# Kernel optimization log

Measured on AMD Instinct MI355X. Metric: run time of the kernel, lower is better.

Reference implementation:

```python
import jax, jax.numpy as jnp
import numpy as np

N, C, H, W = 4, 256, 32, 32
NH = 2                      # att_nhead
HD = C // NH                # 128 per-head dim
MAX_DIS = 7
WS = 2 * MAX_DIS + 1        # 15 window side
WW = WS * WS                # 225 window positions
T = (C / NH) ** 0.5


def _gather_idx(h, w):
    # idx[wpos, m]: flat index into zero-padded (h+14, w+14) grid of the
    # neighbor at window offset wpos for query pixel m (== F.unfold semantics)
    pw = w + 2 * MAX_DIS
    dy, dx = np.meshgrid(np.arange(WS), np.arange(WS), indexing='ij')
    ys, xs = np.meshgrid(np.arange(h), np.arange(w), indexing='ij')
    idx = (dy.reshape(-1, 1) + ys.reshape(1, -1)) * pw + (dx.reshape(-1, 1) + xs.reshape(1, -1))
    return jnp.asarray(idx, dtype=jnp.int32)  # [WW, h*w]


def setup_inputs() -> dict:
    key = jax.random.key(0)
    ks = jax.random.split(key, 14)
    s = 0.02
    return {
        'q': jax.random.normal(ks[0], (N, C, H, W), jnp.float32),
        'k': jax.random.normal(ks[1], (N, C, H, W), jnp.float32),
        'v': jax.random.normal(ks[2], (N, C, H, W), jnp.float32),
        'Wq': jax.random.normal(ks[3], (C, C), jnp.float32) * s,
        'bq': jnp.zeros((C,), jnp.float32),
        'Wk': jax.random.normal(ks[4], (C, C), jnp.float32) * s,
        'bk': jnp.zeros((C,), jnp.float32),
        'Wv': jax.random.normal(ks[5], (C, C), jnp.float32) * s,
        'bv': jnp.zeros((C,), jnp.float32),
        'Wrel': jax.random.normal(ks[6], (NH, WW, HD), jnp.float32) * s,   # grouped 1x1 conv
        'brel': jnp.zeros((NH * WW,), jnp.float32),
        'V_bias': jax.random.normal(ks[7], (NH, HD, WW), jnp.float32) * s,
        'Wfc': jax.random.normal(ks[8], (C, C), jnp.float32) * s,
        'bfc': jnp.zeros((C,), jnp.float32),
    }


def _conv1x1(x, Wt, b):
    return jnp.einsum('nchw,dc->ndhw', x, Wt) + b[None, :, None, None]


def reference(q, k, v, Wq, bq, Wk, bk, Wv, bv, Wrel, brel, V_bias, Wfc, bfc):
    n, c, h, w = q.shape
    hw = h * w
    idx = _gather_idx(h, w)                                   # [WW, hw]
    pad = ((0, 0), (0, 0), (0, 0), (MAX_DIS, MAX_DIS), (MAX_DIS, MAX_DIS))

    q = _conv1x1(q, Wq, bq)
    k = _conv1x1(k, Wk, bk)
    v = _conv1x1(v, Wv, bv)

    # grouped 1x1 conv: relative position logits, [n, NH, WW, hw]
    rel = jnp.einsum('ngcxy,gwc->ngwxy', q.reshape(n, NH, HD, h, w), Wrel)
    rel = rel + brel.reshape(NH, WW)[None, :, :, None, None]
    rel = rel.reshape(n, NH, WW, hw)

    qs = (q / T).reshape(n, NH, HD, hw)

    # unfold K via zero-pad + gather: [n, NH, HD, WW, hw]
    k_pad = jnp.pad(k.reshape(n, NH, HD, h, w), pad).reshape(n, NH, HD, -1)
    k_un = k_pad[..., idx]
    qk = jnp.einsum('ngcm,ngcwm->ngwm', qs, k_un) + rel

    # boundary mask: neighbor inside the original image
    valid = jnp.pad(jnp.ones((h, w), jnp.float32), MAX_DIS).reshape(-1)[idx] > 0
    qk = jnp.where(valid[None, None], qk, jnp.float32(-1e8))
    attn = jax.nn.softmax(qk, axis=2)                         # over window positions

    agg_bias = jnp.einsum('ngwm,gcw->mngc', attn, V_bias).reshape(hw, n, c)

    # local2global scatter + dense einsum == gather of zero-padded V
    v_pad = jnp.pad(v.reshape(n, NH, HD, h, w), pad).reshape(n, NH, HD, -1)
    v_un = v_pad[..., idx]                                    # [n, NH, HD, WW, hw]
    agg_value = jnp.einsum('ngwm,ngcwm->mngc', attn, v_un).reshape(hw, n, c)

    out = (agg_value + agg_bias) @ Wfc.T + bfc                # [hw, n, c]
    return out
```

## Files before the change

kernel.cpp:

```cpp
#include <hip/hip_runtime.h>
#include <math.h>


typedef __attribute__((ext_vector_type(8))) short short8;
typedef __attribute__((ext_vector_type(4))) float floatx4;

__device__ __forceinline__ short f2bf(float f) {
    unsigned u = __float_as_uint(f);
    unsigned r = (u + 0x7fffu + ((u >> 16) & 1u)) >> 16;
    return (short)r;
}
__device__ __forceinline__ float bf2f(short s) {
    return __uint_as_float(((unsigned)(unsigned short)s) << 16);
}

__global__ __launch_bounds__(256)
void conv_kernel(const float* __restrict__ q, const float* __restrict__ k,
                 const float* __restrict__ v,
                 const float* __restrict__ Wq, const float* __restrict__ Wk,
                 const float* __restrict__ Wv, const float* __restrict__ Wfc,
                 const float* __restrict__ Wrel,
                 short* __restrict__ Xhi, short* __restrict__ Xlo,
                 short* __restrict__ Whi, short* __restrict__ Wlo,
                 short* __restrict__ Wrh, short* __restrict__ Wrl)
{
    const int tid = threadIdx.x;
    const int z = blockIdx.z;
    const int lane = tid & 63;
    const int n16 = lane & 15, quad = lane >> 4;

    if (z < 12) {
        __shared__ float st[64 * 33];
        const int sel = z >> 2, batch = z & 3;
        const float* X = (sel == 0 ? q : sel == 1 ? k : v) + ((long)batch << 18);
        const int mb = blockIdx.x, kc = blockIdx.y;
#pragma unroll
        for (int it = 0; it < 8; ++it) {
            int e = tid + it * 256;
            int cc = e >> 6, mm = e & 63;
            st[mm * 33 + cc] = X[((long)(kc * 32 + cc) << 10) + mb * 64 + mm];
        }
        __syncthreads();
        const int mtl = tid >> 6;
        const int m = mtl * 16 + n16;
        short h[8], l[8];
#pragma unroll
        for (int j = 0; j < 8; ++j) {
            float f = st[m * 33 + quad * 8 + j];
            short hb = f2bf(f);
            h[j] = hb;
            l[j] = f2bf(f - bf2f(hb));
        }
        int mt16 = mb * 4 + mtl;
        long off = (long)z * 262144 + (((long)(mt16 * 8 + kc) * 64) + lane) * 8;
        *(short8*)(Xhi + off) = *(short8*)&h[0];
        *(short8*)(Xlo + off) = *(short8*)&l[0];
    } else if (z < 16) {
        if (tid >= 64) return;
        const int w = z - 12;
        const float* W = (w == 0 ? Wq : w == 1 ? Wk : w == 2 ? Wv : Wfc);
        const int dt = blockIdx.x, kc = blockIdx.y;
        const int d = dt * 16 + n16, cb = kc * 32 + quad * 8;
        float4 w0 = *(const float4*)&W[d * 256 + cb];
        float4 w1 = *(const float4*)&W[d * 256 + cb + 4];
        float f[8] = {w0.x, w0.y, w0.z, w0.w, w1.x, w1.y, w1.z, w1.w};
        short h[8], l[8];
#pragma unroll
        for (int j = 0; j < 8; ++j) {
            short hb = f2bf(f[j]);
            h[j] = hb;
            l[j] = f2bf(f[j] - bf2f(hb));
        }
        long off = (long)w * 65536 + (((long)(dt * 8 + kc) * 64) + lane) * 8;
        *(short8*)(Whi + off) = *(short8*)&h[0];
        *(short8*)(Wlo + off) = *(short8*)&l[0];
    } else {
        if (tid >= 64) return;
        const int g = z - 16;
        const int wt = blockIdx.x, kc = blockIdx.y;
        if (wt >= 15 || kc >= 4) return;
        const int w = wt * 16 + n16;
        const int cb = kc * 32 + quad * 8;
        float f[8] = {0.f, 0.f, 0.f, 0.f, 0.f, 0.f, 0.f, 0.f};
        if (w < 225) {
            float4 w0 = *(const float4*)&Wrel[(long)(g * 225 + w) * 128 + cb];
            float4 w1 = *(const float4*)&Wrel[(long)(g * 225 + w) * 128 + cb + 4];
            f[0] = w0.x; f[1] = w0.y; f[2] = w0.z; f[3] = w0.w;
            f[4] = w1.x; f[5] = w1.y; f[6] = w1.z; f[7] = w1.w;
        }
        short h[8], l[8];
#pragma unroll
        for (int j = 0; j < 8; ++j) {
            short hb = f2bf(f[j]);
            h[j] = hb;
            l[j] = f2bf(f[j] - bf2f(hb));
        }
        long off = (long)g * 30720 + (((long)(wt * 4 + kc) * 64) + lane) * 8;
        *(short8*)(Wrh + off) = *(short8*)&h[0];
        *(short8*)(Wrl + off) = *(short8*)&l[0];
    }
}

__global__ __launch_bounds__(256)
void mfma_proj(const short* __restrict__ Xhi, const short* __restrict__ Xlo,
               const short* __restrict__ Whi, const short* __restrict__ Wlo,
               const float* __restrict__ bq, const float* __restrict__ bk,
               const float* __restrict__ bv,
               short* __restrict__ qhi, short* __restrict__ qlo,
               short* __restrict__ khi, short* __restrict__ klo,
               float* __restrict__ vpad)
{
    __shared__ float tile[64 * 65];
    const int tid = threadIdx.x;
    const int wave = tid >> 6, lane = tid & 63;
    const int n16 = lane & 15, quad = lane >> 4;
    const int mb = blockIdx.x, db = blockIdx.y, z = blockIdx.z;
    const int sel = z >> 2, batch = z & 3;
    const int dt = db * 4 + wave;

    const short* Ah = Whi + (long)sel * 65536 + ((long)(dt * 8) * 64 + lane) * 8;
    const short* Al = Wlo + (long)sel * 65536 + ((long)(dt * 8) * 64 + lane) * 8;
    short8 ahi[8], alo[8];
#pragma unroll
    for (int kc = 0; kc < 8; ++kc) {
        ahi[kc] = *(const short8*)(Ah + kc * 512);
        alo[kc] = *(const short8*)(Al + kc * 512);
    }
    const short* Bh = Xhi + (long)z * 262144;
    const short* Bl = Xlo + (long)z * 262144;

    const float* bias = (sel == 0 ? bq : sel == 1 ? bk : bv);
    float4 bv4 = *(const float4*)&bias[dt * 16 + quad * 4];
    float bb[4] = {bv4.x, bv4.y, bv4.z, bv4.w};

    if (sel == 2) {
#pragma unroll
        for (int mtl = 0; mtl < 4; ++mtl) {
            const int mt16 = mb * 4 + mtl;
            floatx4 acc = {0.f, 0.f, 0.f, 0.f};
#pragma unroll
            for (int kc = 0; kc < 8; ++kc) {
                long bo = ((long)(mt16 * 8 + kc) * 64 + lane) * 8;
                short8 bh = *(const short8*)(Bh + bo);
                short8 bl = *(const short8*)(Bl + bo);
                acc = __builtin_amdgcn_mfma_f32_16x16x32_bf16(ahi[kc], bh, acc, 0, 0, 0);
                acc = __builtin_amdgcn_mfma_f32_16x16x32_bf16(ahi[kc], bl, acc, 0, 0, 0);
                acc = __builtin_amdgcn_mfma_f32_16x16x32_bf16(alo[kc], bh, acc, 0, 0, 0);
            }
            const int m = mt16 * 16 + n16;
            float* Y = vpad + (long)batch * 393216;
            const int row = m >> 5, col = (m & 31) + 8;
#pragma unroll
            for (int r = 0; r < 4; ++r)
                Y[(long)(dt * 16 + quad * 4 + r) * 1536 + row * 48 + col] = acc[r] + bb[r];
        }
        return;
    }

#pragma unroll
    for (int mtl = 0; mtl < 4; ++mtl) {
        const int mt16 = mb * 4 + mtl;
        floatx4 acc = {0.f, 0.f, 0.f, 0.f};
#pragma unroll
        for (int kc = 0; kc < 8; ++kc) {
            long bo = ((long)(mt16 * 8 + kc) * 64 + lane) * 8;
            short8 bh = *(const short8*)(Bh + bo);
            short8 bl = *(const short8*)(Bl + bo);
            acc = __builtin_amdgcn_mfma_f32_16x16x32_bf16(ahi[kc], bh, acc, 0, 0, 0);
            acc = __builtin_amdgcn_mfma_f32_16x16x32_bf16(ahi[kc], bl, acc, 0, 0, 0);
            acc = __builtin_amdgcn_mfma_f32_16x16x32_bf16(alo[kc], bh, acc, 0, 0, 0);
        }
        const int ml = mtl * 16 + n16;
        const int cl = wave * 16 + quad * 4;
#pragma unroll
        for (int r = 0; r < 4; ++r)
            tile[ml * 65 + cl + r] = acc[r] + bb[r];
    }
    __syncthreads();

    const float scale = (sel == 1) ? 0.08838834764831845f : 1.0f;
    const int m_l = tid >> 2, c16 = (tid & 3) * 16;
    const int m = mb * 64 + m_l;
    const int cglob = db * 64 + c16;
    const int g = cglob >> 7, ch = cglob & 127;
    const long base = (((long)(batch * 2 + g) << 10) + m) * 128 + ch;
    short h[16], l[16];
#pragma unroll
    for (int j = 0; j < 16; ++j) {
        float f = tile[m_l * 65 + c16 + j] * scale;
        short hb = f2bf(f);
        h[j] = hb;
        l[j] = f2bf(f - bf2f(hb));
    }
    short* oh = sel ? khi : qhi;
    short* ol = sel ? klo : qlo;
    *(short8*)(oh + base)     = *(short8*)&h[0];
    *(short8*)(oh + base + 8) = *(short8*)&h[8];
    *(short8*)(ol + base)     = *(short8*)&l[0];
    *(short8*)(ol + base + 8) = *(short8*)&l[8];
}

__global__ __launch_bounds__(256)
void scores_mfma(const short* __restrict__ qhi, const short* __restrict__ qlo,
                 const short* __restrict__ khi, const short* __restrict__ klo,
                 const short* __restrict__ Wrh, const short* __restrict__ Wrl,
                 const float* __restrict__ brel, float* __restrict__ attn)
{
    __shared__ float qk[16 * 241];
    __shared__ float invl[16];

    const int tid = threadIdx.x;
    const int wave = tid >> 6, lane = tid & 63;
    const int y  = blockIdx.x >> 1;
    const int xt = blockIdx.x & 1;
    const int bz = blockIdx.y;
    const int g = bz & 1;
    const int x0 = xt * 16;
    float* relh = attn + (long)bz * 230400;

    const int n16 = lane & 15, quad = lane >> 4;
    const long qbase = (((long)bz << 10) + y * 32 + x0 + n16) * 128 + quad * 8;
    short8 a_hi[4], a_lo[4];
#pragma unroll
    for (int ch = 0; ch < 4; ++ch) {
        a_hi[ch] = *(const short8*)(qhi + qbase + ch * 32);
        a_lo[ch] = *(const short8*)(qlo + qbase + ch * 32);
    }

    for (int wt = wave; wt < 15; wt += 4) {
        const short* Ah = Wrh + (long)g * 30720 + ((long)(wt * 4) * 64 + lane) * 8;
        const short* Al = Wrl + (long)g * 30720 + ((long)(wt * 4) * 64 + lane) * 8;
        floatx4 racc = {0.f, 0.f, 0.f, 0.f};
#pragma unroll
        for (int kc = 0; kc < 4; ++kc) {
            short8 whh = *(const short8*)(Ah + kc * 512);
            short8 wll = *(const short8*)(Al + kc * 512);
            racc = __builtin_amdgcn_mfma_f32_16x16x32_bf16(whh, a_hi[kc], racc, 0, 0, 0);
            racc = __builtin_amdgcn_mfma_f32_16x16x32_bf16(whh, a_lo[kc], racc, 0, 0, 0);
            racc = __builtin_amdgcn_mfma_f32_16x16x32_bf16(wll, a_hi[kc], racc, 0, 0, 0);
        }
#pragma unroll
        for (int r = 0; r < 4; ++r) {
            int w = wt * 16 + quad * 4 + r;
            if (w < 225) {
                int dy = w / 15, dx = w - dy * 15;
                qk[n16 * 241 + dy * 16 + dx] = racc[r] + brel[g * 225 + w];
            }
        }
    }
    __syncthreads();

    for (int e = tid; e < 16 * 241; e += 256) {
        int px = e / 241, idx = e - px * 241;
        int dy = idx >> 4, dx = idx & 15;
        int hy = y + dy - 7, hx = x0 + px + dx - 7;
        bool valid = (dx < 15) && (dy < 15) &&
                     (hy >= 0) && (hy < 32) && (hx >= 0) && (hx < 32);
        if (!valid) qk[e] = -1e8f;
    }
    __syncthreads();

    for (int dy = wave; dy < 15; dy += 4) {
        const int ky = y + dy - 7;
        if (ky < 0 || ky > 31) continue;
#pragma unroll
        for (int kxt = 0; kxt < 2; ++kxt) {
            const int kxg = x0 - 8 + kxt * 16 + n16;
            const long kb = (((long)bz << 10) + ky * 32 + kxg) * 128 + quad * 8;
            floatx4 acc = {0.f, 0.f, 0.f, 0.f};
#pragma unroll
            for (int ch = 0; ch < 4; ++ch) {
                short8 b_hi = *(const short8*)(khi + kb + ch * 32);
                short8 b_lo = *(const short8*)(klo + kb + ch * 32);
                acc = __builtin_amdgcn_mfma_f32_16x16x32_bf16(a_hi[ch], b_hi, acc, 0, 0, 0);
                acc = __builtin_amdgcn_mfma_f32_16x16x32_bf16(a_hi[ch], b_lo, acc, 0, 0, 0);
                acc = __builtin_amdgcn_mfma_f32_16x16x32_bf16(a_lo[ch], b_hi, acc, 0, 0, 0);
            }
            if (kxg >= 0 && kxg < 32) {
#pragma unroll
                for (int r = 0; r < 4; ++r) {
                    int m = quad * 4 + r;
                    int dx = kxg - (x0 + m) + 7;
                    if (dx >= 0 && dx < 15) {
                        int s = m * 241 + dy * 16 + dx;
                        qk[s] = qk[s] + acc[r];
                    }
                }
            }
        }
    }
    __syncthreads();

    {
        int px = tid >> 4, s = tid & 15;
        float mx = -3.0e38f;
        for (int w = s; w < 240; w += 16) mx = fmaxf(mx, qk[px * 241 + w]);
#pragma unroll
        for (int msk = 8; msk; msk >>= 1) mx = fmaxf(mx, __shfl_xor(mx, msk));
        float sum = 0.f;
        for (int w = s; w < 240; w += 16) {
            float p = __expf(qk[px * 241 + w] - mx);
            qk[px * 241 + w] = p;
            sum += p;
        }
#pragma unroll
        for (int msk = 8; msk; msk >>= 1) sum += __shfl_xor(sum, msk);
        if (s == 0) invl[px] = 1.0f / sum;
    }
    __syncthreads();

    for (int e = tid; e < 3600; e += 256) {
        int px = e & 15, w = e >> 4;
        int dy2 = w / 15, dx2 = w - dy2 * 15;
        relh[((long)w << 10) + y * 32 + x0 + px] =
            qk[px * 241 + dy2 * 16 + dx2] * invl[px];
    }
}

__global__ __launch_bounds__(256)
void pv_kernel(const float* __restrict__ vpad, const float* __restrict__ attn,
               const float* __restrict__ Vbias,
               short* __restrict__ AGhi, short* __restrict__ AGlo)
{
    __shared__ __align__(16) float pa[225 * 32];
    const int tid = threadIdx.x;
    const int y   = blockIdx.x;
    const int chh = blockIdx.y;
    const int bz  = blockIdx.z;
    const int n = bz >> 1, g = bz & 1;

    const float* ab = attn + (long)bz * 230400 + y * 32;
    for (int e = tid; e < 1800; e += 256) {
        int w = e >> 3, x4 = (e & 7) * 4;
        *(float4*)&pa[w * 32 + x4] = *(const float4*)&ab[((long)w << 10) + x4];
    }
    __syncthreads();

    const int chg = tid >> 3;
    const int xq  = tid & 7;
    const int c0  = chh * 64 + chg * 2;
    const int x0  = xq * 4;
    const float* v0 = vpad + (long)bz * 196608 + (long)c0 * 1536;
    const float* v1 = v0 + 1536;
    const float* b0 = Vbias + (g * 128 + c0) * 225;
    const float* b1 = b0 + 225;

    float acc0[4] = {0.f, 0.f, 0.f, 0.f};
    float acc1[4] = {0.f, 0.f, 0.f, 0.f};

    for (int dy = 0; dy < 15; ++dy) {
        int hy = y + dy - 7;
        if (hy < 0 || hy > 31) continue;
        const float4* r0 = (const float4*)(v0 + hy * 48 + x0);
        const float4* r1 = (const float4*)(v1 + hy * 48 + x0);
        float wa[20], wb[20];
#pragma unroll
        for (int t = 0; t < 5; ++t) {
            float4 a = r0[t], b = r1[t];
            wa[4*t+0] = a.x; wa[4*t+1] = a.y; wa[4*t+2] = a.z; wa[4*t+3] = a.w;
            wb[4*t+0] = b.x; wb[4*t+1] = b.y; wb[4*t+2] = b.z; wb[4*t+3] = b.w;
        }
        const float* par = &pa[dy * 15 * 32 + x0];
        const float* vb0 = b0 + dy * 15;
        const float* vb1 = b1 + dy * 15;
#pragma unroll
        for (int dx = 0; dx < 15; ++dx) {
            float4 p4 = *(const float4*)&par[dx * 32];
            float ba = vb0[dx], bb = vb1[dx];
            acc0[0] += p4.x * (wa[1 + dx] + ba);
            acc0[1] += p4.y * (wa[2 + dx] + ba);
            acc0[2] += p4.z * (wa[3 + dx] + ba);
            acc0[3] += p4.w * (wa[4 + dx] + ba);
            acc1[0] += p4.x * (wb[1 + dx] + bb);
            acc1[1] += p4.y * (wb[2 + dx] + bb);
            acc1[2] += p4.z * (wb[3 + dx] + bb);
            acc1[3] += p4.w * (wb[4 + dx] + bb);
        }
    }
    __syncthreads();

    float* tile = pa;
#pragma unroll
    for (int i = 0; i < 4; ++i) {
        tile[(x0 + i) * 65 + chg * 2 + 0] = acc0[i];
        tile[(x0 + i) * 65 + chg * 2 + 1] = acc1[i];
    }
    __syncthreads();

    const int lane = tid & 63, sub = tid >> 6;
    const int kcp = sub & 1, mtp = sub >> 1;
    const int n16 = lane & 15, quad = lane >> 4;
    const int m_loc = mtp * 16 + n16;
    const int c_loc = kcp * 32 + quad * 8;
    short h[8], l[8];
#pragma unroll
    for (int j = 0; j < 8; ++j) {
        float f = tile[m_loc * 65 + c_loc + j];
        short hb = f2bf(f);
        h[j] = hb;
        l[j] = f2bf(f - bf2f(hb));
    }
    const int mt16 = y * 2 + mtp;
    const int kc = g * 4 + chh * 2 + kcp;
    long off = (long)n * 262144 + (((long)(mt16 * 8 + kc) * 64) + lane) * 8;
    *(short8*)(AGhi + off) = *(short8*)&h[0];
    *(short8*)(AGlo + off) = *(short8*)&l[0];
}

__global__ __launch_bounds__(256)
void mfma_fc(const short* __restrict__ Ahi, const short* __restrict__ Alo,
             const short* __restrict__ Whi, const short* __restrict__ Wlo,
             const float* __restrict__ bfc, float* __restrict__ out)
{
    __shared__ float tile[64 * 68];
    const int tid = threadIdx.x;
    const int wave = tid >> 6, lane = tid & 63;
    const int n16 = lane & 15, quad = lane >> 4;
    const int mb = blockIdx.x, db = blockIdx.y, nz = blockIdx.z;
    const int dt = db * 4 + wave;

    const short* Ah = Whi + (long)3 * 65536 + ((long)(dt * 8) * 64 + lane) * 8;
    const short* Al = Wlo + (long)3 * 65536 + ((long)(dt * 8) * 64 + lane) * 8;
    short8 ahi[8], alo[8];
#pragma unroll
    for (int kc = 0; kc < 8; ++kc) {
        ahi[kc] = *(const short8*)(Ah + kc * 512);
        alo[kc] = *(const short8*)(Al + kc * 512);
    }
    const short* Bh = Ahi + (long)nz * 262144;
    const short* Bl = Alo + (long)nz * 262144;

    float4 bv4 = *(const float4*)&bfc[dt * 16 + quad * 4];
    float bb[4] = {bv4.x, bv4.y, bv4.z, bv4.w};

#pragma unroll
    for (int mtl = 0; mtl < 4; ++mtl) {
        const int mt16 = mb * 4 + mtl;
        floatx4 acc = {0.f, 0.f, 0.f, 0.f};
#pragma unroll
        for (int kc = 0; kc < 8; ++kc) {
            long bo = ((long)(mt16 * 8 + kc) * 64 + lane) * 8;
            short8 bh = *(const short8*)(Bh + bo);
            short8 bl = *(const short8*)(Bl + bo);
            acc = __builtin_amdgcn_mfma_f32_16x16x32_bf16(ahi[kc], bh, acc, 0, 0, 0);
            acc = __builtin_amdgcn_mfma_f32_16x16x32_bf16(ahi[kc], bl, acc, 0, 0, 0);
            acc = __builtin_amdgcn_mfma_f32_16x16x32_bf16(alo[kc], bh, acc, 0, 0, 0);
        }
        const int ml = mtl * 16 + n16;
        const int dl = wave * 16 + quad * 4;
#pragma unroll
        for (int r = 0; r < 4; ++r)
            tile[ml * 68 + dl + r] = acc[r] + bb[r];
    }
    __syncthreads();
#pragma unroll
    for (int it = 0; it < 16; ++it) {
        int e = tid + it * 256;
        int dd = e & 63, mm = e >> 6;
        out[(long)(mb * 64 + mm) * 1024 + nz * 256 + db * 64 + dd] = tile[mm * 68 + dd];
    }
}

extern "C" void kernel_launch(void* const* d_in, const int* in_sizes, int n_in,
                              void* d_out, int out_size, void* d_ws, size_t ws_size,
                              hipStream_t stream)
{
    const float* q    = (const float*)d_in[0];
    const float* k    = (const float*)d_in[1];
    const float* v    = (const float*)d_in[2];
    const float* Wq   = (const float*)d_in[3];
    const float* bq   = (const float*)d_in[4];
    const float* Wk   = (const float*)d_in[5];
    const float* bk   = (const float*)d_in[6];
    const float* Wv   = (const float*)d_in[7];
    const float* bv   = (const float*)d_in[8];
    const float* Wrel = (const float*)d_in[9];
    const float* brel = (const float*)d_in[10];
    const float* Vb   = (const float*)d_in[11];
    const float* Wfc  = (const float*)d_in[12];
    const float* bfc  = (const float*)d_in[13];
    float* out = (float*)d_out;

    float* ws   = (float*)d_ws;
    float* vpad = ws + 2097152;
    float* attn = ws + 4718592;
    short* qhi  = (short*)(ws + 6561792);
    short* qlo  = (short*)(ws + 7086080);
    short* khi  = (short*)(ws + 7610368);
    short* klo  = (short*)(ws + 8134656);
    short* Xhi  = (short*)(ws + 8658944);
    short* Xlo  = (short*)(ws + 10231808);
    short* Whi  = (short*)(ws + 11804672);
    short* Wlo  = (short*)(ws + 11935744);
    short* AGhi = (short*)(ws + 12066816);
    short* AGlo = (short*)(ws + 12591104);
    short* Wrh  = (short*)(ws + 13115392);
    short* Wrl  = (short*)(ws + 13146112);

    dim3 blk(256);

    hipMemsetAsync(vpad, 0, (size_t)1572864 * 4, stream);

    conv_kernel<<<dim3(16, 8, 18), blk, 0, stream>>>(q, k, v, Wq, Wk, Wv, Wfc,
                                                     Wrel, Xhi, Xlo, Whi, Wlo,
                                                     Wrh, Wrl);

    mfma_proj<<<dim3(16, 4, 12), blk, 0, stream>>>(Xhi, Xlo, Whi, Wlo,
                                                   bq, bk, bv,
                                                   qhi, qlo, khi, klo, vpad);

    scores_mfma<<<dim3(64, 8), blk, 0, stream>>>(qhi, qlo, khi, klo,
                                                 Wrh, Wrl, brel, attn);

    pv_kernel<<<dim3(32, 2, 8), blk, 0, stream>>>(vpad, attn, Vb, AGhi, AGlo);

    mfma_fc<<<dim3(16, 4, 4), blk, 0, stream>>>(AGhi, AGlo, Whi, Wlo, bfc, out);
}
```

Measured before the change: 174.0 us.

## Fuse softmax scores with PV aggregation and zero V padding in projection

Merges the scores/softmax kernel and the PV aggregation kernel into one launch. Normalized attention now stays in shared memory instead of a global attn buffer written and re-read. Each block now covers 16 pixels and all 128 channels of one head rather than 32 pixels and 64 channels, which changes the per-block work balance. The padding columns of vpad are zeroed inside the projection kernel, replacing a separate full memset.

```diff
diff --git a/kernel.cpp b/kernel.cpp
--- a/kernel.cpp
+++ b/kernel.cpp
@@ -154,6 +154,15 @@
             for (int r = 0; r < 4; ++r)
                 Y[(long)(dt * 16 + quad * 4 + r) * 1536 + row * 48 + col] = acc[r] + bb[r];
         }
+        {
+            float* Y = vpad + (long)batch * 393216;
+            const int ch_l = tid >> 2, rest = tid & 3;
+            const int prow = rest >> 1, side = rest & 1;
+            long po = (long)(db * 64 + ch_l) * 1536 + (mb * 2 + prow) * 48 + side * 40;
+            float4 z4 = make_float4(0.f, 0.f, 0.f, 0.f);
+            *(float4*)&Y[po] = z4;
+            *(float4*)&Y[po + 4] = z4;
+        }
         return;
     }
 
@@ -201,12 +210,15 @@
 }
 
 __global__ __launch_bounds__(256)
-void scores_mfma(const short* __restrict__ qhi, const short* __restrict__ qlo,
-                 const short* __restrict__ khi, const short* __restrict__ klo,
-                 const short* __restrict__ Wrh, const short* __restrict__ Wrl,
-                 const float* __restrict__ brel, float* __restrict__ attn)
+void scores_pv(const short* __restrict__ qhi, const short* __restrict__ qlo,
+               const short* __restrict__ khi, const short* __restrict__ klo,
+               const short* __restrict__ Wrh, const short* __restrict__ Wrl,
+               const float* __restrict__ brel,
+               const float* __restrict__ vpad, const float* __restrict__ Vbias,
+               short* __restrict__ AGhi, short* __restrict__ AGlo)
 {
     __shared__ float qk[16 * 241];
+    __shared__ __align__(16) float pa[225 * 16];
     __shared__ float invl[16];
 
     const int tid = threadIdx.x;
@@ -214,9 +226,8 @@
     const int y  = blockIdx.x >> 1;
     const int xt = blockIdx.x & 1;
     const int bz = blockIdx.y;
-    const int g = bz & 1;
+    const int n = bz >> 1, g = bz & 1;
     const int x0 = xt * 16;
-    float* relh = attn + (long)bz * 230400;
 
     const int n16 = lane & 15, quad = lane >> 4;
     const long qbase = (((long)bz << 10) + y * 32 + x0 + n16) * 128 + quad * 8;
@@ -312,34 +323,15 @@
     for (int e = tid; e < 3600; e += 256) {
         int px = e & 15, w = e >> 4;
         int dy2 = w / 15, dx2 = w - dy2 * 15;
-        relh[((long)w << 10) + y * 32 + x0 + px] =
-            qk[px * 241 + dy2 * 16 + dx2] * invl[px];
-    }
-}
-
-__global__ __launch_bounds__(256)
-void pv_kernel(const float* __restrict__ vpad, const float* __restrict__ attn,
-               const float* __restrict__ Vbias,
-               short* __restrict__ AGhi, short* __restrict__ AGlo)
-{
-    __shared__ __align__(16) float pa[225 * 32];
-    const int tid = threadIdx.x;
-    const int y   = blockIdx.x;
-    const int chh = blockIdx.y;
-    const int bz  = blockIdx.z;
-    const int n = bz >> 1, g = bz & 1;
-
-    const float* ab = attn + (long)bz * 230400 + y * 32;
-    for (int e = tid; e < 1800; e += 256) {
-        int w = e >> 3, x4 = (e & 7) * 4;
-        *(float4*)&pa[w * 32 + x4] = *(const float4*)&ab[((long)w << 10) + x4];
-    }
-    __syncthreads();
-
-    const int chg = tid >> 3;
-    const int xq  = tid & 7;
-    const int c0  = chh * 64 + chg * 2;
-    const int x0  = xq * 4;
+        pa[w * 16 + px] = qk[px * 241 + dy2 * 16 + dx2] * invl[px];
+    }
+    __syncthreads();
+
+    const int chg = tid >> 2;
+    const int xq  = tid & 3;
+    const int c0  = chg * 2;
+    const int x0l = xq * 4;
+    const int x0g = x0 + x0l;
     const float* v0 = vpad + (long)bz * 196608 + (long)c0 * 1536;
     const float* v1 = v0 + 1536;
     const float* b0 = Vbias + (g * 128 + c0) * 225;
@@ -351,8 +343,8 @@
     for (int dy = 0; dy < 15; ++dy) {
         int hy = y + dy - 7;
         if (hy < 0 || hy > 31) continue;
-        const float4* r0 = (const float4*)(v0 + hy * 48 + x0);
-        const float4* r1 = (const float4*)(v1 + hy * 48 + x0);
+        const float4* r0 = (const float4*)(v0 + hy * 48 + x0g);
+        const float4* r1 = (const float4*)(v1 + hy * 48 + x0g);
         float wa[20], wb[20];
 #pragma unroll
         for (int t = 0; t < 5; ++t) {
@@ -360,12 +352,12 @@
             wa[4*t+0] = a.x; wa[4*t+1] = a.y; wa[4*t+2] = a.z; wa[4*t+3] = a.w;
             wb[4*t+0] = b.x; wb[4*t+1] = b.y; wb[4*t+2] = b.z; wb[4*t+3] = b.w;
         }
-        const float* par = &pa[dy * 15 * 32 + x0];
+        const float* par = &pa[dy * 15 * 16 + x0l];
         const float* vb0 = b0 + dy * 15;
         const float* vb1 = b1 + dy * 15;
 #pragma unroll
         for (int dx = 0; dx < 15; ++dx) {
-            float4 p4 = *(const float4*)&par[dx * 32];
+            float4 p4 = *(const float4*)&par[dx * 16];
             float ba = vb0[dx], bb = vb1[dx];
             acc0[0] += p4.x * (wa[1 + dx] + ba);
             acc0[1] += p4.y * (wa[2 + dx] + ba);
@@ -379,29 +371,26 @@
     }
     __syncthreads();
 
-    float* tile = pa;
+    float* tile = qk;
 #pragma unroll
     for (int i = 0; i < 4; ++i) {
-        tile[(x0 + i) * 65 + chg * 2 + 0] = acc0[i];
-        tile[(x0 + i) * 65 + chg * 2 + 1] = acc1[i];
-    }
-    __syncthreads();
-
-    const int lane = tid & 63, sub = tid >> 6;
-    const int kcp = sub & 1, mtp = sub >> 1;
-    const int n16 = lane & 15, quad = lane >> 4;
-    const int m_loc = mtp * 16 + n16;
+        tile[(x0l + i) * 129 + c0 + 0] = acc0[i];
+        tile[(x0l + i) * 129 + c0 + 1] = acc1[i];
+    }
+    __syncthreads();
+
+    const int kcp = tid >> 6;
     const int c_loc = kcp * 32 + quad * 8;
     short h[8], l[8];
 #pragma unroll
     for (int j = 0; j < 8; ++j) {
-        float f = tile[m_loc * 65 + c_loc + j];
+        float f = tile[n16 * 129 + c_loc + j];
         short hb = f2bf(f);
         h[j] = hb;
         l[j] = f2bf(f - bf2f(hb));
     }
-    const int mt16 = y * 2 + mtp;
-    const int kc = g * 4 + chh * 2 + kcp;
+    const int mt16 = y * 2 + xt;
+    const int kc = g * 4 + kcp;
     long off = (long)n * 262144 + (((long)(mt16 * 8 + kc) * 64) + lane) * 8;
     *(short8*)(AGhi + off) = *(short8*)&h[0];
     *(short8*)(AGlo + off) = *(short8*)&l[0];
@@ -483,7 +472,6 @@
 
     float* ws   = (float*)d_ws;
     float* vpad = ws + 2097152;
-    float* attn = ws + 4718592;
     short* qhi  = (short*)(ws + 6561792);
     short* qlo  = (short*)(ws + 7086080);
     short* khi  = (short*)(ws + 7610368);
@@ -499,8 +487,6 @@
 
     dim3 blk(256);
 
-    hipMemsetAsync(vpad, 0, (size_t)1572864 * 4, stream);
-
     conv_kernel<<<dim3(16, 8, 18), blk, 0, stream>>>(q, k, v, Wq, Wk, Wv, Wfc,
                                                      Wrel, Xhi, Xlo, Whi, Wlo,
                                                      Wrh, Wrl);
@@ -509,10 +495,9 @@
                                                    bq, bk, bv,
                                                    qhi, qlo, khi, klo, vpad);
 
-    scores_mfma<<<dim3(64, 8), blk, 0, stream>>>(qhi, qlo, khi, klo,
-                                                 Wrh, Wrl, brel, attn);
-
-    pv_kernel<<<dim3(32, 2, 8), blk, 0, stream>>>(vpad, attn, Vb, AGhi, AGlo);
+    scores_pv<<<dim3(64, 8), blk, 0, stream>>>(qhi, qlo, khi, klo,
+                                               Wrh, Wrl, brel, vpad, Vb,
+                                               AGhi, AGlo);
 
     mfma_fc<<<dim3(16, 4, 4), blk, 0, stream>>>(AGhi, AGlo, Whi, Wlo, bfc, out);
 }
```

Result: slower. 178.1 us (+2.4%).

## Split projection and FC GEMMs into 16-row blocks and drop vpad memset

Applied to the files above, without the earlier changes.

The mfma_proj and mfma_fc kernels now give each block a single 16-row M tile instead of four. The grid grows fourfold, and weight fragments are loaded inside the k-loop instead of held in 16 register vectors. The FC epilogue becomes one float4 store per thread, and the q/k epilogue writes 4-element vectors. The separate hipMemsetAsync on the padded V buffer is removed; the V-projection blocks now write zeros into the horizontal padding columns themselves. The aim is better occupancy and one less memset. The cost is reloading weights once per M tile, plus smaller, less efficient stores.

```diff
diff --git a/kernel.cpp b/kernel.cpp
--- a/kernel.cpp
+++ b/kernel.cpp
@@ -3,6 +3,7 @@
 
 
 typedef __attribute__((ext_vector_type(8))) short short8;
+typedef __attribute__((ext_vector_type(4))) short short4v;
 typedef __attribute__((ext_vector_type(4))) float floatx4;
 
 __device__ __forceinline__ short f2bf(float f) {
@@ -110,22 +111,16 @@
                short* __restrict__ khi, short* __restrict__ klo,
                float* __restrict__ vpad)
 {
-    __shared__ float tile[64 * 65];
+    __shared__ float tile[16 * 65];
     const int tid = threadIdx.x;
     const int wave = tid >> 6, lane = tid & 63;
     const int n16 = lane & 15, quad = lane >> 4;
-    const int mb = blockIdx.x, db = blockIdx.y, z = blockIdx.z;
+    const int mt16 = blockIdx.x, db = blockIdx.y, z = blockIdx.z;
     const int sel = z >> 2, batch = z & 3;
     const int dt = db * 4 + wave;
 
     const short* Ah = Whi + (long)sel * 65536 + ((long)(dt * 8) * 64 + lane) * 8;
     const short* Al = Wlo + (long)sel * 65536 + ((long)(dt * 8) * 64 + lane) * 8;
-    short8 ahi[8], alo[8];
-#pragma unroll
-    for (int kc = 0; kc < 8; ++kc) {
-        ahi[kc] = *(const short8*)(Ah + kc * 512);
-        alo[kc] = *(const short8*)(Al + kc * 512);
-    }
     const short* Bh = Xhi + (long)z * 262144;
     const short* Bl = Xlo + (long)z * 262144;
 
@@ -133,60 +128,51 @@
     float4 bv4 = *(const float4*)&bias[dt * 16 + quad * 4];
     float bb[4] = {bv4.x, bv4.y, bv4.z, bv4.w};
 
+    floatx4 acc = {0.f, 0.f, 0.f, 0.f};
+#pragma unroll
+    for (int kc = 0; kc < 8; ++kc) {
+        short8 ahi = *(const short8*)(Ah + kc * 512);
+        short8 alo = *(const short8*)(Al + kc * 512);
+        long bo = ((long)(mt16 * 8 + kc) * 64 + lane) * 8;
+        short8 bh = *(const short8*)(Bh + bo);
+        short8 bl = *(const short8*)(Bl + bo);
+        acc = __builtin_amdgcn_mfma_f32_16x16x32_bf16(ahi, bh, acc, 0, 0, 0);
+        acc = __builtin_amdgcn_mfma_f32_16x16x32_bf16(ahi, bl, acc, 0, 0, 0);
+        acc = __builtin_amdgcn_mfma_f32_16x16x32_bf16(alo, bh, acc, 0, 0, 0);
+    }
+
     if (sel == 2) {
-#pragma unroll
-        for (int mtl = 0; mtl < 4; ++mtl) {
-            const int mt16 = mb * 4 + mtl;
-            floatx4 acc = {0.f, 0.f, 0.f, 0.f};
-#pragma unroll
-            for (int kc = 0; kc < 8; ++kc) {
-                long bo = ((long)(mt16 * 8 + kc) * 64 + lane) * 8;
-                short8 bh = *(const short8*)(Bh + bo);
-                short8 bl = *(const short8*)(Bl + bo);
-                acc = __builtin_amdgcn_mfma_f32_16x16x32_bf16(ahi[kc], bh, acc, 0, 0, 0);
-                acc = __builtin_amdgcn_mfma_f32_16x16x32_bf16(ahi[kc], bl, acc, 0, 0, 0);
-                acc = __builtin_amdgcn_mfma_f32_16x16x32_bf16(alo[kc], bh, acc, 0, 0, 0);
-            }
-            const int m = mt16 * 16 + n16;
-            float* Y = vpad + (long)batch * 393216;
-            const int row = m >> 5, col = (m & 31) + 8;
-#pragma unroll
-            for (int r = 0; r < 4; ++r)
-                Y[(long)(dt * 16 + quad * 4 + r) * 1536 + row * 48 + col] = acc[r] + bb[r];
+        const int m = mt16 * 16 + n16;
+        float* Y = vpad + (long)batch * 393216;
+        const int row = m >> 5, col = (m & 31) + 8;
+#pragma unroll
+        for (int r = 0; r < 4; ++r)
+            Y[(long)(dt * 16 + quad * 4 + r) * 1536 + row * 48 + col] = acc[r] + bb[r];
+        {
+            const int prow = mt16 >> 1, side = mt16 & 1;
+            const int ch_l = tid >> 2, f2 = (tid & 3) * 2;
+            long po = (long)(db * 64 + ch_l) * 1536 + prow * 48 + side * 40 + f2;
+            Y[po] = 0.f;
+            Y[po + 1] = 0.f;
         }
         return;
     }
 
-#pragma unroll
-    for (int mtl = 0; mtl < 4; ++mtl) {
-        const int mt16 = mb * 4 + mtl;
-        floatx4 acc = {0.f, 0.f, 0.f, 0.f};
-#pragma unroll
-        for (int kc = 0; kc < 8; ++kc) {
-            long bo = ((long)(mt16 * 8 + kc) * 64 + lane) * 8;
-            short8 bh = *(const short8*)(Bh + bo);
-            short8 bl = *(const short8*)(Bl + bo);
-            acc = __builtin_amdgcn_mfma_f32_16x16x32_bf16(ahi[kc], bh, acc, 0, 0, 0);
-            acc = __builtin_amdgcn_mfma_f32_16x16x32_bf16(ahi[kc], bl, acc, 0, 0, 0);
-            acc = __builtin_amdgcn_mfma_f32_16x16x32_bf16(alo[kc], bh, acc, 0, 0, 0);
-        }
-        const int ml = mtl * 16 + n16;
-        const int cl = wave * 16 + quad * 4;
-#pragma unroll
-        for (int r = 0; r < 4; ++r)
-            tile[ml * 65 + cl + r] = acc[r] + bb[r];
-    }
+    const int cl = wave * 16 + quad * 4;
+#pragma unroll
+    for (int r = 0; r < 4; ++r)
+        tile[n16 * 65 + cl + r] = acc[r] + bb[r];
     __syncthreads();
 
     const float scale = (sel == 1) ? 0.08838834764831845f : 1.0f;
-    const int m_l = tid >> 2, c16 = (tid & 3) * 16;
-    const int m = mb * 64 + m_l;
+    const int m_l = tid >> 4, c16 = (tid & 15) * 4;
+    const int m = mt16 * 16 + m_l;
     const int cglob = db * 64 + c16;
     const int g = cglob >> 7, ch = cglob & 127;
     const long base = (((long)(batch * 2 + g) << 10) + m) * 128 + ch;
-    short h[16], l[16];
-#pragma unroll
-    for (int j = 0; j < 16; ++j) {
+    short h[4], l[4];
+#pragma unroll
+    for (int j = 0; j < 4; ++j) {
         float f = tile[m_l * 65 + c16 + j] * scale;
         short hb = f2bf(f);
         h[j] = hb;
@@ -194,10 +180,8 @@
     }
     short* oh = sel ? khi : qhi;
     short* ol = sel ? klo : qlo;
-    *(short8*)(oh + base)     = *(short8*)&h[0];
-    *(short8*)(oh + base + 8) = *(short8*)&h[8];
-    *(short8*)(ol + base)     = *(short8*)&l[0];
-    *(short8*)(ol + base + 8) = *(short8*)&l[8];
+    *(short4v*)(oh + base) = *(short4v*)&h[0];
+    *(short4v*)(ol + base) = *(short4v*)&l[0];
 }
 
 __global__ __launch_bounds__(256)
@@ -412,53 +396,43 @@
              const short* __restrict__ Whi, const short* __restrict__ Wlo,
              const float* __restrict__ bfc, float* __restrict__ out)
 {
-    __shared__ float tile[64 * 68];
+    __shared__ float tile[16 * 68];
     const int tid = threadIdx.x;
     const int wave = tid >> 6, lane = tid & 63;
     const int n16 = lane & 15, quad = lane >> 4;
-    const int mb = blockIdx.x, db = blockIdx.y, nz = blockIdx.z;
+    const int mt16 = blockIdx.x, db = blockIdx.y, nz = blockIdx.z;
     const int dt = db * 4 + wave;
 
     const short* Ah = Whi + (long)3 * 65536 + ((long)(dt * 8) * 64 + lane) * 8;
     const short* Al = Wlo + (long)3 * 65536 + ((long)(dt * 8) * 64 + lane) * 8;
-    short8 ahi[8], alo[8];
-#pragma unroll
-    for (int kc = 0; kc < 8; ++kc) {
-        ahi[kc] = *(const short8*)(Ah + kc * 512);
-        alo[kc] = *(const short8*)(Al + kc * 512);
-    }
     const short* Bh = Ahi + (long)nz * 262144;
     const short* Bl = Alo + (long)nz * 262144;
 
     float4 bv4 = *(const float4*)&bfc[dt * 16 + quad * 4];
     float bb[4] = {bv4.x, bv4.y, bv4.z, bv4.w};
 
-#pragma unroll
-    for (int mtl = 0; mtl < 4; ++mtl) {
-        const int mt16 = mb * 4 + mtl;
-        floatx4 acc = {0.f, 0.f, 0.f, 0.f};
-#pragma unroll
-        for (int kc = 0; kc < 8; ++kc) {
-            long bo = ((long)(mt16 * 8 + kc) * 64 + lane) * 8;
-            short8 bh = *(const short8*)(Bh + bo);
-            short8 bl = *(const short8*)(Bl + bo);
-            acc = __builtin_amdgcn_mfma_f32_16x16x32_bf16(ahi[kc], bh, acc, 0, 0, 0);
-            acc = __builtin_amdgcn_mfma_f32_16x16x32_bf16(ahi[kc], bl, acc, 0, 0, 0);
-            acc = __builtin_amdgcn_mfma_f32_16x16x32_bf16(alo[kc], bh, acc, 0, 0, 0);
-        }
-        const int ml = mtl * 16 + n16;
-        const int dl = wave * 16 + quad * 4;
-#pragma unroll
-        for (int r = 0; r < 4; ++r)
-            tile[ml * 68 + dl + r] = acc[r] + bb[r];
-    }
-    __syncthreads();
-#pragma unroll
-    for (int it = 0; it < 16; ++it) {
-        int e = tid + it * 256;
-        int dd = e & 63, mm = e >> 6;
-        out[(long)(mb * 64 + mm) * 1024 + nz * 256 + db * 64 + dd] = tile[mm * 68 + dd];
-    }
+    floatx4 acc = {0.f, 0.f, 0.f, 0.f};
+#pragma unroll
+    for (int kc = 0; kc < 8; ++kc) {
+        short8 ahi = *(const short8*)(Ah + kc * 512);
+        short8 alo = *(const short8*)(Al + kc * 512);
+        long bo = ((long)(mt16 * 8 + kc) * 64 + lane) * 8;
+        short8 bh = *(const short8*)(Bh + bo);
+        short8 bl = *(const short8*)(Bl + bo);
+        acc = __builtin_amdgcn_mfma_f32_16x16x32_bf16(ahi, bh, acc, 0, 0, 0);
+        acc = __builtin_amdgcn_mfma_f32_16x16x32_bf16(ahi, bl, acc, 0, 0, 0);
+        acc = __builtin_amdgcn_mfma_f32_16x16x32_bf16(alo, bh, acc, 0, 0, 0);
+    }
+
+    const int dl = wave * 16 + quad * 4;
+#pragma unroll
+    for (int r = 0; r < 4; ++r)
+        tile[n16 * 68 + dl + r] = acc[r] + bb[r];
+    __syncthreads();
+
+    const int mm = tid >> 4, d4 = (tid & 15) * 4;
+    float4 o4 = *(const float4*)&tile[mm * 68 + d4];
+    *(float4*)&out[(long)(mt16 * 16 + mm) * 1024 + nz * 256 + db * 64 + d4] = o4;
 }
 
 extern "C" void kernel_launch(void* const* d_in, const int* in_sizes, int n_in,
@@ -499,13 +473,11 @@
 
     dim3 blk(256);
 
-    hipMemsetAsync(vpad, 0, (size_t)1572864 * 4, stream);
-
     conv_kernel<<<dim3(16, 8, 18), blk, 0, stream>>>(q, k, v, Wq, Wk, Wv, Wfc,
                                                      Wrel, Xhi, Xlo, Whi, Wlo,
                                                      Wrh, Wrl);
 
-    mfma_proj<<<dim3(16, 4, 12), blk, 0, stream>>>(Xhi, Xlo, Whi, Wlo,
+    mfma_proj<<<dim3(64, 4, 12), blk, 0, stream>>>(Xhi, Xlo, Whi, Wlo,
                                                    bq, bk, bv,
                                                    qhi, qlo, khi, klo, vpad);
 
@@ -514,5 +486,5 @@
 
     pv_kernel<<<dim3(32, 2, 8), blk, 0, stream>>>(vpad, attn, Vb, AGhi, AGlo);
 
-    mfma_fc<<<dim3(16, 4, 4), blk, 0, stream>>>(AGhi, AGlo, Whi, Wlo, bfc, out);
-}
+    mfma_fc<<<dim3(64, 4, 4), blk, 0, stream>>>(AGhi, AGlo, Whi, Wlo, bfc, out);
+}
```

After: 167.7 us. 1.04x faster.
